# Optimization experiments

Measured on AMD Instinct MI355X. Metric: run time of the kernel, lower is better.

Reference implementation:

```python
import jax, jax.numpy as jnp
import numpy as np

EPSILON = 0.1
ALPHA = 0.5
N_ITER = 10
B, N, D, N_USERS = 4096, 4096, 16, 100000


def setup_inputs() -> dict:
    key = jax.random.key(0)
    k1, k2, k3, k4, k5, k6 = jax.random.split(key, 6)
    users_tensor = jax.random.randint(k1, (B,), 0, N_USERS)
    pois_tensor = jax.random.randint(k2, (B, N), 0, N)
    D_tensor = jax.random.uniform(k3, (B, N), dtype=jnp.float32)
    # ScaledEmbedding: normal init scaled by 1/embedding_dim
    poi_emb = jax.random.normal(k4, (N, D), dtype=jnp.float32) / D
    user_emb = jax.random.normal(k5, (N_USERS, D), dtype=jnp.float32) / D
    capacities = jax.random.uniform(k6, (N,), dtype=jnp.float32) + 0.5
    return {"users_tensor": users_tensor, "pois_tensor": pois_tensor,
            "D_tensor": D_tensor, "poi_emb": poi_emb,
            "user_emb": user_emb, "capacities": capacities}


def reference(users_tensor, pois_tensor, D_tensor, poi_emb, user_emb, capacities):
    pe = poi_emb[pois_tensor]            # [B, N, D]
    ue = user_emb[users_tensor]          # [B, D]
    dot = jnp.einsum('bnd,bd->bn', pe, ue)   # [B, N]
    affinity = (1.0 - ALPHA) * dot - ALPHA * (D_tensor / jnp.mean(D_tensor))
    K = jnp.exp(affinity / EPSILON)      # [B, N]
    a = jnp.ones((B,), dtype=K.dtype)
    b = capacities

    def body(i, uv):
        u, v = uv
        u = a / (K @ v)        # [B]
        v = b / (K.T @ u)      # [N]
        return (u, v)

    u0 = jnp.ones((B,), dtype=K.dtype)
    v0 = jnp.ones((N,), dtype=K.dtype)
    u, v = jax.lax.fori_loop(0, N_ITER, body, (u0, v0))
    P = K * (u[:, None] * v[None, :])    # [B, N]
    return P
```

## Files before the change

### kernel.cpp

```cpp
#include <hip/hip_runtime.h>
#include <hip/hip_fp16.h>

#define BB 4096
#define NN 4096
#define RPB 4
#define RPI 8
#define NBLK (BB / RPI)
#define NTSLOT 60

__device__ __forceinline__ int swzK(int bid) { return (bid & 7) * 128 + (bid >> 3); }

typedef float vf4 __attribute__((ext_vector_type(4)));
typedef int   vi4 __attribute__((ext_vector_type(4)));
typedef float fv2 __attribute__((ext_vector_type(2)));
__device__ __forceinline__ float4 ntl4(const float4* p) {
    vf4 r = __builtin_nontemporal_load((const vf4*)p);
    return *(float4*)&r;
}
__device__ __forceinline__ int4 ntl4i(const int4* p) {
    vi4 r = __builtin_nontemporal_load((const vi4*)p);
    return *(int4*)&r;
}
__device__ __forceinline__ void nts4(float4* p, float4 v) {
    __builtin_nontemporal_store(*(vf4*)&v, (vf4*)p);
}

__device__ __forceinline__ void dec4(int w, float* f) {
    fv2 lo = __builtin_amdgcn_cvt_pk_f32_fp8(w, false);
    fv2 hi = __builtin_amdgcn_cvt_pk_f32_fp8(w, true);
    f[0] = lo.x; f[1] = lo.y; f[2] = hi.x; f[3] = hi.y;
}

__global__ __launch_bounds__(256) void k_mean(
        const float* __restrict__ Dt, float* __restrict__ dsum,
        float* __restrict__ v) {
    const int tid = blockIdx.x * blockDim.x + threadIdx.x;
    const int gs = gridDim.x * blockDim.x;
    if (tid < NN) v[tid] = 1.0f;
    const float4* D4 = (const float4*)Dt;
    const int total4 = (BB * NN) / 4;
    float s = 0.f;
    for (int i = tid; i < total4; i += gs) {
        float4 d = ntl4(&D4[i]);
        s += (d.x + d.y) + (d.z + d.w);
    }
    #pragma unroll
    for (int off = 32; off > 0; off >>= 1) s += __shfl_down(s, off, 64);
    __shared__ float ls[4];
    if ((threadIdx.x & 63) == 0) ls[threadIdx.x >> 6] = s;
    __syncthreads();
    if (threadIdx.x == 0) atomicAdd(dsum, (ls[0] + ls[1]) + (ls[2] + ls[3]));
}

__global__ __launch_bounds__(256) void k_K(
        const int* __restrict__ users, const int* __restrict__ pois,
        const float* __restrict__ Dt, const float* __restrict__ poi_emb,
        const float* __restrict__ user_emb, const float* __restrict__ dsum,
        __half* __restrict__ K, unsigned char* __restrict__ K8) {
    __shared__ __half slut[RPB][NN];
    __shared__ float ues[RPB * 16];
    const int t = threadIdx.x;
    const int b0 = swzK(blockIdx.x) * RPB;
    if (t < RPB * 16) {
        int r = t >> 4, d = t & 15;
        ues[t] = user_emb[(size_t)users[b0 + r] * 16 + d];
    }
    __syncthreads();
    float ue[RPB][16];
    #pragma unroll
    for (int r = 0; r < RPB; r++)
        #pragma unroll
        for (int d = 0; d < 16; d++) ue[r][d] = ues[r * 16 + d];

    const float4* pe4 = (const float4*)poi_emb;
    for (int j = t; j < NN; j += 256) {
        float4 p0 = pe4[j * 4 + 0];
        float4 p1 = pe4[j * 4 + 1];
        float4 p2 = pe4[j * 4 + 2];
        float4 p3 = pe4[j * 4 + 3];
        #pragma unroll
        for (int r = 0; r < RPB; r++) {
            float acc = p0.x*ue[r][0]  + p0.y*ue[r][1]  + p0.z*ue[r][2]  + p0.w*ue[r][3]
                      + p1.x*ue[r][4]  + p1.y*ue[r][5]  + p1.z*ue[r][6]  + p1.w*ue[r][7]
                      + p2.x*ue[r][8]  + p2.y*ue[r][9]  + p2.z*ue[r][10] + p2.w*ue[r][11]
                      + p3.x*ue[r][12] + p3.y*ue[r][13] + p3.z*ue[r][14] + p3.w*ue[r][15];
            slut[r][j] = __float2half(acc);
        }
    }
    __syncthreads();
    const float cc = 5.0f * 16777216.0f / dsum[0];
    #pragma unroll
    for (int r = 0; r < RPB; r++) {
        const size_t base = (size_t)(b0 + r) * NN;
        const int4*   p4 = (const int4*)(pois + base);
        const float4* d4 = (const float4*)(Dt + base);
        #pragma unroll
        for (int i = 0; i < NN / 4 / 256; i++) {
            const int q = t + i * 256;
            int4   ci = ntl4i(&p4[q]);
            float4 cd = ntl4(&d4[q]);
            float k0 = __expf(5.0f * __half2float(slut[r][ci.x]) - cc * cd.x);
            float k1 = __expf(5.0f * __half2float(slut[r][ci.y]) - cc * cd.y);
            float k2 = __expf(5.0f * __half2float(slut[r][ci.z]) - cc * cd.z);
            float k3 = __expf(5.0f * __half2float(slut[r][ci.w]) - cc * cd.w);
            __half2* kw = (__half2*)&K[base + 4 * (size_t)q];
            kw[0] = __floats2half2_rn(k0, k1);
            kw[1] = __floats2half2_rn(k2, k3);
            int w8 = __builtin_amdgcn_cvt_pk_fp8_f32(16.f * k0, 16.f * k1, 0, false);
            w8 = __builtin_amdgcn_cvt_pk_fp8_f32(16.f * k2, 16.f * k3, w8, true);
            ((int*)(K8 + base))[q] = w8;
        }
    }
}

__global__ __launch_bounds__(512) void k_it(
        const unsigned char* __restrict__ K8, const float* __restrict__ v,
        float* __restrict__ part, float* __restrict__ u) {
    const int t = threadIdx.x;
    const int sb = (blockIdx.x & 7) * 64 + (blockIdx.x >> 3);
    const int r0 = sb * RPI;

    const float4* w4 = (const float4*)v;
    float4 w0 = w4[2 * t], w1 = w4[2 * t + 1];

    uint2 h8[RPI];
    #pragma unroll
    for (int r = 0; r < RPI; r++)
        h8[r] = ((const uint2*)(K8 + (size_t)(r0 + r) * NN))[t];

    float acc[RPI];
    #pragma unroll
    for (int r = 0; r < RPI; r++) {
        float f[8];
        dec4((int)h8[r].x, f);
        dec4((int)h8[r].y, f + 4);
        acc[r] = f[0]*w0.x + f[1]*w0.y + f[2]*w0.z + f[3]*w0.w
               + f[4]*w1.x + f[5]*w1.y + f[6]*w1.z + f[7]*w1.w;
    }
    #pragma unroll
    for (int off = 32; off > 0; off >>= 1)
        #pragma unroll
        for (int r = 0; r < RPI; r++) acc[r] += __shfl_down(acc[r], off, 64);
    __shared__ float ls[8][RPI];
    __shared__ float us[RPI];
    if ((t & 63) == 0)
        #pragma unroll
        for (int r = 0; r < RPI; r++) ls[t >> 6][r] = acc[r];
    __syncthreads();
    if (t < RPI) {
        float s = 0.f;
        #pragma unroll
        for (int wv = 0; wv < 8; wv++) s += ls[wv][t];
        float uu = 1.0f / s;
        us[t] = uu;
        u[r0 + t] = 16.0f * uu;
    }
    __syncthreads();

    float4 A0 = make_float4(0, 0, 0, 0), A1 = A0;
    #pragma unroll
    for (int r = 0; r < RPI; r++) {
        const float ur = us[r];
        float f[8];
        dec4((int)h8[r].x, f);
        dec4((int)h8[r].y, f + 4);
        A0.x += ur * f[0]; A0.y += ur * f[1]; A0.z += ur * f[2]; A0.w += ur * f[3];
        A1.x += ur * f[4]; A1.y += ur * f[5]; A1.z += ur * f[6]; A1.w += ur * f[7];
    }
    float4* p4 = (float4*)(part + (size_t)sb * NN);
    nts4(&p4[2 * t],     A0);
    nts4(&p4[2 * t + 1], A1);
}

__global__ __launch_bounds__(256) void k_red(
        const float* __restrict__ part, const float* __restrict__ cap,
        float* __restrict__ v) {
    const int t = threadIdx.x;
    const int g = blockIdx.x;
    const int j = t & 7;
    const int s = t >> 3;
    const float4* p4 = (const float4*)part;
    float4 a = make_float4(0, 0, 0, 0);
    #pragma unroll
    for (int i = 0; i < NBLK / 32; i++) {
        float4 x = ntl4(&p4[(size_t)(s + 32 * i) * (NN / 4) + g * 8 + j]);
        a.x += x.x; a.y += x.y; a.z += x.z; a.w += x.w;
    }
    __shared__ float4 red[32][8];
    red[s][j] = a;
    __syncthreads();
    if (t < 8) {
        float4 b = red[0][t];
        #pragma unroll
        for (int s2 = 1; s2 < 32; s2++) {
            float4 x = red[s2][t];
            b.x += x.x; b.y += x.y; b.z += x.z; b.w += x.w;
        }
        float4 cc = ((const float4*)cap)[g * 8 + t];
        ((float4*)v)[g * 8 + t] =
            make_float4(cc.x / b.x, cc.y / b.y, cc.z / b.z, cc.w / b.w);
    }
}

__global__ __launch_bounds__(256) void k_P(
        const __half* __restrict__ K, const float* __restrict__ u,
        const float* __restrict__ v, float* __restrict__ P) {
    const int t = threadIdx.x;
    const int slot = blockIdx.x >> 3;
    const int sb = (blockIdx.x & 7) * 64 + slot;
    const int r0 = sb * RPI;
    const bool nt = (slot >= NTSLOT);
    const float4* v4 = (const float4*)v;
    float4 va0 = v4[2 * t],       va1 = v4[2 * t + 1];
    float4 vb0 = v4[512 + 2 * t], vb1 = v4[512 + 2 * t + 1];
    #pragma unroll 2
    for (int r = 0; r < RPI; r++) {
        const int b = r0 + r;
        const float ub = u[b];
        const size_t base = (size_t)b * NN;
        const float4* k4 = (const float4*)(K + base);
        float4 raw0 = nt ? ntl4(&k4[t])       : k4[t];
        float4 raw1 = nt ? ntl4(&k4[256 + t]) : k4[256 + t];
        const __half2* ha = (const __half2*)&raw0;
        const __half2* hb = (const __half2*)&raw1;
        float2 f0 = __half22float2(ha[0]);
        float2 f1 = __half22float2(ha[1]);
        float2 f2 = __half22float2(ha[2]);
        float2 f3 = __half22float2(ha[3]);
        float2 g0 = __half22float2(hb[0]);
        float2 g1 = __half22float2(hb[1]);
        float2 g2 = __half22float2(hb[2]);
        float2 g3 = __half22float2(hb[3]);
        float4* P4 = (float4*)(P + base);
        nts4(&P4[2*t],       make_float4(f0.x*ub*va0.x, f0.y*ub*va0.y, f1.x*ub*va0.z, f1.y*ub*va0.w));
        nts4(&P4[2*t+1],     make_float4(f2.x*ub*va1.x, f2.y*ub*va1.y, f3.x*ub*va1.z, f3.y*ub*va1.w));
        nts4(&P4[512+2*t],   make_float4(g0.x*ub*vb0.x, g0.y*ub*vb0.y, g1.x*ub*vb0.z, g1.y*ub*vb0.w));
        nts4(&P4[512+2*t+1], make_float4(g2.x*ub*vb1.x, g2.y*ub*vb1.y, g3.x*ub*vb1.z, g3.y*ub*vb1.w));
    }
}

extern "C" void kernel_launch(void* const* d_in, const int* in_sizes, int n_in,
                              void* d_out, int out_size, void* d_ws, size_t ws_size,
                              hipStream_t stream) {
    const int*   users    = (const int*)d_in[0];
    const int*   pois     = (const int*)d_in[1];
    const float* Dt       = (const float*)d_in[2];
    const float* poi_emb  = (const float*)d_in[3];
    const float* user_emb = (const float*)d_in[4];
    const float* cap      = (const float*)d_in[5];
    float* out = (float*)d_out;

    float*  wsf  = (float*)d_ws;
    float*  dsum = wsf;
    float*  u    = wsf + 64;
    float*  v    = wsf + 64 + BB;
    __half* Kh   = (__half*)(wsf + 64 + BB + NN);
    float*  part = (float*)d_out;
    unsigned char* K8 = (unsigned char*)(part + (size_t)NBLK * NN);

    (void)hipMemsetAsync(dsum, 0, sizeof(float), stream);
    k_mean<<<2048, 256, 0, stream>>>(Dt, dsum, v);
    k_K<<<BB / RPB, 256, 0, stream>>>(users, pois, Dt, poi_emb, user_emb, dsum, Kh, K8);
    for (int it = 0; it < 10; it++) {
        k_it<<<NBLK, 512, 0, stream>>>(K8, v, part, u);
        k_red<<<128, 256, 0, stream>>>(part, cap, v);
    }
    k_P<<<NBLK, 256, 0, stream>>>(Kh, u, v, out);
}
```

Baseline: 372.8 us.

## Process 16 rows per iteration block and use nontemporal stores for K writes

The Sinkhorn iteration kernel now uses 1024-thread blocks that each cover 16 rows. The two half-blocks' column partials are summed in shared memory before one partial row per block is written, which halves the partial-sum buffer and the work in the reduction kernel. The K-building kernel now writes its fp16 and fp8 copies with nontemporal stores. In exchange there is an extra LDS exchange and barrier, fewer and larger blocks per launch, and possible occupancy limits from the 1024-thread launch bound.

Result: faster. 358.4 us (-3.9%).

```diff
diff --git a/kernel.cpp b/kernel.cpp
--- a/kernel.cpp
+++ b/kernel.cpp
@@ -4,13 +4,16 @@
 #define BB 4096
 #define NN 4096
 #define RPB 4
-#define RPI 8
-#define NBLK (BB / RPI)
+#define RPI 16
+#define IBLK (BB / RPI)
+#define NSL IBLK
+#define RPP 8
 #define NTSLOT 60
 
 __device__ __forceinline__ int swzK(int bid) { return (bid & 7) * 128 + (bid >> 3); }
 
 typedef float vf4 __attribute__((ext_vector_type(4)));
+typedef float vf2 __attribute__((ext_vector_type(2)));
 typedef int   vi4 __attribute__((ext_vector_type(4)));
 typedef float fv2 __attribute__((ext_vector_type(2)));
 __device__ __forceinline__ float4 ntl4(const float4* p) {
@@ -23,6 +26,9 @@
 }
 __device__ __forceinline__ void nts4(float4* p, float4 v) {
     __builtin_nontemporal_store(*(vf4*)&v, (vf4*)p);
+}
+__device__ __forceinline__ void nts2(float2* p, float2 v) {
+    __builtin_nontemporal_store(*(vf2*)&v, (vf2*)p);
 }
 
 __device__ __forceinline__ void dec4(int w, float* f) {
@@ -103,34 +109,39 @@
             float k1 = __expf(5.0f * __half2float(slut[r][ci.y]) - cc * cd.y);
             float k2 = __expf(5.0f * __half2float(slut[r][ci.z]) - cc * cd.z);
             float k3 = __expf(5.0f * __half2float(slut[r][ci.w]) - cc * cd.w);
-            __half2* kw = (__half2*)&K[base + 4 * (size_t)q];
-            kw[0] = __floats2half2_rn(k0, k1);
-            kw[1] = __floats2half2_rn(k2, k3);
+            __half2 ha = __floats2half2_rn(k0, k1);
+            __half2 hb = __floats2half2_rn(k2, k3);
+            float2 w16;
+            *(__half2*)&w16.x = ha;
+            *(__half2*)&w16.y = hb;
+            nts2((float2*)&K[base + 4 * (size_t)q], w16);
             int w8 = __builtin_amdgcn_cvt_pk_fp8_f32(16.f * k0, 16.f * k1, 0, false);
             w8 = __builtin_amdgcn_cvt_pk_fp8_f32(16.f * k2, 16.f * k3, w8, true);
-            ((int*)(K8 + base))[q] = w8;
+            __builtin_nontemporal_store(w8, &((int*)(K8 + base))[q]);
         }
     }
 }
 
-__global__ __launch_bounds__(512) void k_it(
+__global__ __launch_bounds__(1024) void k_it(
         const unsigned char* __restrict__ K8, const float* __restrict__ v,
         float* __restrict__ part, float* __restrict__ u) {
     const int t = threadIdx.x;
-    const int sb = (blockIdx.x & 7) * 64 + (blockIdx.x >> 3);
-    const int r0 = sb * RPI;
+    const int c = t & 511;
+    const int rh = t >> 9;
+    const int sb = (blockIdx.x & 7) * 32 + (blockIdx.x >> 3);
+    const int r0 = sb * RPI + rh * 8;
 
     const float4* w4 = (const float4*)v;
-    float4 w0 = w4[2 * t], w1 = w4[2 * t + 1];
-
-    uint2 h8[RPI];
-    #pragma unroll
-    for (int r = 0; r < RPI; r++)
-        h8[r] = ((const uint2*)(K8 + (size_t)(r0 + r) * NN))[t];
-
-    float acc[RPI];
-    #pragma unroll
-    for (int r = 0; r < RPI; r++) {
+    float4 w0 = w4[2 * c], w1 = w4[2 * c + 1];
+
+    uint2 h8[8];
+    #pragma unroll
+    for (int r = 0; r < 8; r++)
+        h8[r] = ((const uint2*)(K8 + (size_t)(r0 + r) * NN))[c];
+
+    float acc[8];
+    #pragma unroll
+    for (int r = 0; r < 8; r++) {
         float f[8];
         dec4((int)h8[r].x, f);
         dec4((int)h8[r].y, f + 4);
@@ -140,36 +151,46 @@
     #pragma unroll
     for (int off = 32; off > 0; off >>= 1)
         #pragma unroll
-        for (int r = 0; r < RPI; r++) acc[r] += __shfl_down(acc[r], off, 64);
-    __shared__ float ls[8][RPI];
-    __shared__ float us[RPI];
+        for (int r = 0; r < 8; r++) acc[r] += __shfl_down(acc[r], off, 64);
+    __shared__ float ls[16][8];
+    __shared__ float us[16];
     if ((t & 63) == 0)
         #pragma unroll
-        for (int r = 0; r < RPI; r++) ls[t >> 6][r] = acc[r];
-    __syncthreads();
-    if (t < RPI) {
+        for (int r = 0; r < 8; r++) ls[t >> 6][r] = acc[r];
+    __syncthreads();
+    if (t < 16) {
+        const int wb = (t < 8) ? 0 : 8;
+        const int rr = (t < 8) ? t : (t - 8);
         float s = 0.f;
         #pragma unroll
-        for (int wv = 0; wv < 8; wv++) s += ls[wv][t];
+        for (int wv = 0; wv < 8; wv++) s += ls[wb + wv][rr];
         float uu = 1.0f / s;
         us[t] = uu;
-        u[r0 + t] = 16.0f * uu;
+        u[sb * RPI + t] = 16.0f * uu;
     }
     __syncthreads();
 
     float4 A0 = make_float4(0, 0, 0, 0), A1 = A0;
     #pragma unroll
-    for (int r = 0; r < RPI; r++) {
-        const float ur = us[r];
+    for (int r = 0; r < 8; r++) {
+        const float ur = us[rh * 8 + r];
         float f[8];
         dec4((int)h8[r].x, f);
         dec4((int)h8[r].y, f + 4);
         A0.x += ur * f[0]; A0.y += ur * f[1]; A0.z += ur * f[2]; A0.w += ur * f[3];
         A1.x += ur * f[4]; A1.y += ur * f[5]; A1.z += ur * f[6]; A1.w += ur * f[7];
     }
-    float4* p4 = (float4*)(part + (size_t)sb * NN);
-    nts4(&p4[2 * t],     A0);
-    nts4(&p4[2 * t + 1], A1);
+    __shared__ float4 ps[512][2];
+    if (rh == 1) { ps[c][0] = A0; ps[c][1] = A1; }
+    __syncthreads();
+    if (rh == 0) {
+        float4 B0 = ps[c][0], B1 = ps[c][1];
+        A0.x += B0.x; A0.y += B0.y; A0.z += B0.z; A0.w += B0.w;
+        A1.x += B1.x; A1.y += B1.y; A1.z += B1.z; A1.w += B1.w;
+        float4* p4 = (float4*)(part + (size_t)sb * NN);
+        nts4(&p4[2 * c],     A0);
+        nts4(&p4[2 * c + 1], A1);
+    }
 }
 
 __global__ __launch_bounds__(256) void k_red(
@@ -182,7 +203,7 @@
     const float4* p4 = (const float4*)part;
     float4 a = make_float4(0, 0, 0, 0);
     #pragma unroll
-    for (int i = 0; i < NBLK / 32; i++) {
+    for (int i = 0; i < NSL / 32; i++) {
         float4 x = ntl4(&p4[(size_t)(s + 32 * i) * (NN / 4) + g * 8 + j]);
         a.x += x.x; a.y += x.y; a.z += x.z; a.w += x.w;
     }
@@ -208,13 +229,13 @@
     const int t = threadIdx.x;
     const int slot = blockIdx.x >> 3;
     const int sb = (blockIdx.x & 7) * 64 + slot;
-    const int r0 = sb * RPI;
+    const int r0 = sb * RPP;
     const bool nt = (slot >= NTSLOT);
     const float4* v4 = (const float4*)v;
     float4 va0 = v4[2 * t],       va1 = v4[2 * t + 1];
     float4 vb0 = v4[512 + 2 * t], vb1 = v4[512 + 2 * t + 1];
     #pragma unroll 2
-    for (int r = 0; r < RPI; r++) {
+    for (int r = 0; r < RPP; r++) {
         const int b = r0 + r;
         const float ub = u[b];
         const size_t base = (size_t)b * NN;
@@ -256,14 +277,14 @@
     float*  v    = wsf + 64 + BB;
     __half* Kh   = (__half*)(wsf + 64 + BB + NN);
     float*  part = (float*)d_out;
-    unsigned char* K8 = (unsigned char*)(part + (size_t)NBLK * NN);
+    unsigned char* K8 = (unsigned char*)(part + (size_t)NSL * NN);
 
     (void)hipMemsetAsync(dsum, 0, sizeof(float), stream);
     k_mean<<<2048, 256, 0, stream>>>(Dt, dsum, v);
     k_K<<<BB / RPB, 256, 0, stream>>>(users, pois, Dt, poi_emb, user_emb, dsum, Kh, K8);
     for (int it = 0; it < 10; it++) {
-        k_it<<<NBLK, 512, 0, stream>>>(K8, v, part, u);
+        k_it<<<IBLK, 1024, 0, stream>>>(K8, v, part, u);
         k_red<<<128, 256, 0, stream>>>(part, cap, v);
     }
-    k_P<<<NBLK, 256, 0, stream>>>(Kh, u, v, out);
-}
+    k_P<<<BB / RPP, 256, 0, stream>>>(Kh, u, v, out);
+}
```
